# Performance work log

Measured on AMD Instinct MI355X. Metric: run time of the kernel, lower is better.

## Reference

```python
import jax, jax.numpy as jnp
import numpy as np

DIM = 1024
EXPANSION = 4
NUM_EXPERTS = 8
N_TOKENS = 4096
CAPACITY_FACTOR = 1.0  # also becomes the gate's k -> top-1 (bug-faithful)
EPS = 1e-6


def setup_inputs() -> dict:
    key = jax.random.key(0)
    ks = jax.random.split(key, 7)
    h = DIM * EXPANSION
    s = 0.02
    return {
        "x": jax.random.normal(ks[0], (N_TOKENS, DIM), dtype=jnp.float32),
        "w_gate": jax.random.normal(ks[1], (DIM, NUM_EXPERTS), dtype=jnp.float32) * s,
        "b_gate": jnp.zeros((NUM_EXPERTS,), dtype=jnp.float32),
        "w1": jax.random.normal(ks[2], (NUM_EXPERTS, DIM, h), dtype=jnp.float32) * s,
        "b1": jnp.zeros((NUM_EXPERTS, h), dtype=jnp.float32),
        "w2": jax.random.normal(ks[3], (NUM_EXPERTS, h, DIM), dtype=jnp.float32) * s,
        "b2": jnp.zeros((NUM_EXPERTS, DIM), dtype=jnp.float32),
    }


def fast_gelu(x):
    return x * jax.nn.sigmoid(1.702 * x)


def switch_gate(x, w_gate, b_gate):
    # x: [n, d] -> gate_scores: [n, e]
    gate_scores = jax.nn.softmax(x @ w_gate + b_gate, axis=-1)
    capacity = int(CAPACITY_FACTOR * x.shape[0])
    k = int(CAPACITY_FACTOR)  # SwitchMoE passes capacity_factor as k -> top-1
    _, top_k_idx = jax.lax.top_k(gate_scores, k)  # [n, k]
    mask = jnp.zeros_like(gate_scores).at[
        jnp.arange(x.shape[0])[:, None], top_k_idx
    ].set(1.0)
    masked = gate_scores * mask
    denom = masked.sum(axis=0, keepdims=True) + EPS  # [1, e]
    gate_scores = masked / denom * capacity
    # aux loss (use_aux_loss=True in SwitchMoE)
    load = gate_scores.sum(axis=0)               # [e]
    importance = gate_scores.sum(axis=1).mean()  # scalar
    loss = jnp.mean((load - importance) ** 2)
    return gate_scores, loss


def reference(x, w_gate, b_gate, w1, b1, w2, b2):
    gate_scores, loss = switch_gate(x, w_gate, b_gate)  # [n, e], scalar
    # dense compute-all-experts (faithful to the naive module)
    h = fast_gelu(jnp.einsum("nd,edh->enh", x, w1) + b1[:, None, :])  # [e, n, h]
    expert_out = jnp.einsum("enh,ehd->end", h, w2) + b2[:, None, :]   # [e, n, d]
    # weighted combine: sum_e gate[n,e] * expert_out[e,n,d]
    moe_output = jnp.einsum("ne,end->nd", gate_scores, expert_out)
    return moe_output, loss
```

## Files before the change

### kernel.cpp

```cpp
#include <hip/hip_runtime.h>
#include <hip/hip_bf16.h>
#include <math.h>

#define DIMK   1024
#define HDIM   4096
#define NEXP   8
#define NTOK   4096
#define EPSV   1e-6f

typedef __attribute__((ext_vector_type(4))) float  f32x4;
typedef __attribute__((ext_vector_type(8))) __bf16 bf16x8;
typedef __attribute__((ext_vector_type(4))) __bf16 bf16x4;

__device__ __forceinline__ __bf16 f2bf(float f) { return (__bf16)f; }

__global__ void init_kernel(int* counts, int* cursors, float* S) {
    int t = threadIdx.x;
    if (t < NEXP) { counts[t] = 0; cursors[t] = 0; S[t] = 0.0f; }
}

__global__ __launch_bounds__(256) void gate_kernel(
    const float* __restrict__ x, const float* __restrict__ wg,
    const float* __restrict__ bg,
    float* S, int* counts, float* score_top, int* texp)
{
    int wave = threadIdx.x >> 6;
    int lane = threadIdx.x & 63;
    int n = blockIdx.x * 4 + wave;
    const float* xr = x + (size_t)n * DIMK;

    float acc[NEXP];
#pragma unroll
    for (int e = 0; e < NEXP; e++) acc[e] = 0.0f;

    for (int d = lane; d < DIMK; d += 64) {
        float xv = xr[d];
        const float* wr = wg + (size_t)d * NEXP;
#pragma unroll
        for (int e = 0; e < NEXP; e++) acc[e] += xv * wr[e];
    }
#pragma unroll
    for (int e = 0; e < NEXP; e++) {
#pragma unroll
        for (int off = 32; off > 0; off >>= 1)
            acc[e] += __shfl_down(acc[e], off, 64);
    }
    if (lane == 0) {
        float l[NEXP];
        float m = -1e30f;
#pragma unroll
        for (int e = 0; e < NEXP; e++) { l[e] = acc[e] + bg[e]; m = fmaxf(m, l[e]); }
        float p[NEXP]; float s = 0.0f;
#pragma unroll
        for (int e = 0; e < NEXP; e++) { p[e] = expf(l[e] - m); s += p[e]; }
        int best = 0; float bv = p[0];
#pragma unroll
        for (int e = 1; e < NEXP; e++) if (p[e] > bv) { bv = p[e]; best = e; }
        float sc = bv / s;
        score_top[n] = sc;
        texp[n] = best;
        atomicAdd(&S[best], sc);
        atomicAdd(&counts[best], 1);
    }
}

__global__ void finalize_kernel(const float* S, const int* counts,
                                int* offsets, float* loss_out)
{
    if (threadIdx.x == 0 && blockIdx.x == 0) {
        int off = 0;
        float loadv[NEXP]; float tot = 0.0f;
        for (int e = 0; e < NEXP; e++) { offsets[e] = off; off += counts[e]; }
        for (int e = 0; e < NEXP; e++) {
            loadv[e] = S[e] / (S[e] + EPSV) * (float)NTOK;
            tot += loadv[e];
        }
        float imp = tot / (float)NTOK;
        float loss = 0.0f;
        for (int e = 0; e < NEXP; e++) { float d = loadv[e] - imp; loss += d * d; }
        loss_out[0] = loss / (float)NEXP;
    }
}

__global__ __launch_bounds__(256) void assign_kernel(
    const int* __restrict__ texp, const float* __restrict__ score_top,
    const float* __restrict__ S, const int* __restrict__ offsets,
    int* cursors, int* perm, float* gatew)
{
    int n = blockIdx.x * 256 + threadIdx.x;
    int e = texp[n];
    int pos = atomicAdd(&cursors[e], 1);
    perm[offsets[e] + pos] = n;
    gatew[n] = score_top[n] / (S[e] + EPSV) * (float)NTOK;
}

__global__ __launch_bounds__(256) void gemm1_kernel(
    const float* __restrict__ x, const float* __restrict__ w1,
    const float* __restrict__ b1,
    const int* __restrict__ perm, const int* __restrict__ counts,
    const int* __restrict__ offsets, __bf16* __restrict__ hbuf)
{
    int bx  = blockIdx.x;
    int e   = bx >> 10;
    int rem = bx & 1023;
    int mt  = rem >> 5;
    int nt  = rem & 31;
    int ce  = counts[e];
    int m0  = mt * 128;
    if (m0 >= ce) return;
    int off = offsets[e];
    int n0  = nt * 128;
    const float* B = w1 + (size_t)e * DIMK * HDIM;

    __shared__ __bf16 As[128][40];
    __shared__ __bf16 Bs[128][40];

    int t = threadIdx.x;

    const float* aptr[4];
#pragma unroll
    for (int i = 0; i < 4; i++) {
        int r  = (t >> 3) + 32 * i;
        int ri = m0 + r; if (ri >= ce) ri = ce - 1;
        aptr[i] = x + (size_t)perm[off + ri] * DIMK;
    }
    int ac4 = (t & 7) * 4;

    int bj = t & 127;
    int bgp = t >> 7;
    const float* bcol = B + n0 + bj;

    int lane = t & 63;
    int wv   = t >> 6;
    int wm   = (wv >> 1) * 64;
    int wn   = (wv & 1) * 64;
    int lr   = lane & 15;
    int lq   = lane >> 4;

    f32x4 acc[4][4];
#pragma unroll
    for (int mi = 0; mi < 4; mi++)
#pragma unroll
        for (int ni = 0; ni < 4; ni++) acc[mi][ni] = (f32x4)0.0f;

    for (int k0 = 0; k0 < DIMK; k0 += 32) {
#pragma unroll
        for (int i = 0; i < 4; i++) {
            int r = (t >> 3) + 32 * i;
            f32x4 v = *(const f32x4*)(aptr[i] + k0 + ac4);
            bf16x4 s4 = { f2bf(v.x), f2bf(v.y), f2bf(v.z), f2bf(v.w) };
            *(bf16x4*)&As[r][ac4] = s4;
        }
#pragma unroll
        for (int i = 0; i < 4; i++) {
            int kk = bgp * 4 + i * 8;
            const float* p = bcol + (size_t)(k0 + kk) * HDIM;
            bf16x4 s4 = { f2bf(p[0]), f2bf(p[HDIM]),
                          f2bf(p[2 * HDIM]), f2bf(p[3 * HDIM]) };
            *(bf16x4*)&Bs[bj][kk] = s4;
        }
        __syncthreads();

        bf16x8 af[4], bfr[4];
#pragma unroll
        for (int i = 0; i < 4; i++) {
            af[i]  = *(const bf16x8*)&As[wm + i * 16 + lr][lq * 8];
            bfr[i] = *(const bf16x8*)&Bs[wn + i * 16 + lr][lq * 8];
        }
#pragma unroll
        for (int mi = 0; mi < 4; mi++)
#pragma unroll
            for (int ni = 0; ni < 4; ni++)
                acc[mi][ni] = __builtin_amdgcn_mfma_f32_16x16x32_bf16(
                    af[mi], bfr[ni], acc[mi][ni], 0, 0, 0);
        __syncthreads();
    }

    const float* b1e = b1 + (size_t)e * HDIM;
#pragma unroll
    for (int mi = 0; mi < 4; mi++) {
#pragma unroll
        for (int r = 0; r < 4; r++) {
            int i = m0 + wm + mi * 16 + lq * 4 + r;
            if (i < ce) {
                __bf16* hrow = hbuf + (size_t)(off + i) * HDIM;
#pragma unroll
                for (int ni = 0; ni < 4; ni++) {
                    int j = n0 + wn + ni * 16 + lr;
                    float v = acc[mi][ni][r] + b1e[j];
                    v = v / (1.0f + __expf(-1.702f * v));
                    hrow[j] = f2bf(v);
                }
            }
        }
    }
}

__global__ __launch_bounds__(256) void gemm2_kernel(
    const __bf16* __restrict__ hbuf, const float* __restrict__ w2,
    const float* __restrict__ b2,
    const int* __restrict__ perm, const int* __restrict__ counts,
    const int* __restrict__ offsets, const float* __restrict__ gatew,
    float* __restrict__ out)
{
    int bx  = blockIdx.x;
    int e   = bx >> 9;
    int rem = bx & 511;
    int mt  = rem >> 3;
    int nt  = rem & 7;
    int ce  = counts[e];
    int m0  = mt * 64;
    if (m0 >= ce) return;
    int off = offsets[e];
    int n0  = nt * 128;
    const float* B = w2 + (size_t)e * HDIM * DIMK;

    __shared__ __bf16 As[64][40];
    __shared__ __bf16 Bs[128][40];

    int t = threadIdx.x;

    int ar = t >> 2;
    int ac8 = (t & 3) * 8;
    {
        int ri = m0 + ar; if (ri >= ce) ri = ce - 1;
        ar = ar;
    }
    int ri0 = m0 + ar; if (ri0 >= ce) ri0 = ce - 1;
    const __bf16* aptr = hbuf + (size_t)(off + ri0) * HDIM;

    int bj = t & 127;
    int bgp = t >> 7;
    const float* bcol = B + n0 + bj;

    int lane = t & 63;
    int wv   = t >> 6;
    int wm   = (wv >> 1) * 32;
    int wn   = (wv & 1) * 64;
    int lr   = lane & 15;
    int lq   = lane >> 4;

    f32x4 acc[2][4];
#pragma unroll
    for (int mi = 0; mi < 2; mi++)
#pragma unroll
        for (int ni = 0; ni < 4; ni++) acc[mi][ni] = (f32x4)0.0f;

    for (int k0 = 0; k0 < HDIM; k0 += 32) {
        {
            bf16x8 v = *(const bf16x8*)(aptr + k0 + ac8);
            *(bf16x8*)&As[ar][ac8] = v;
        }
#pragma unroll
        for (int i = 0; i < 4; i++) {
            int kk = bgp * 4 + i * 8;
            const float* p = bcol + (size_t)(k0 + kk) * DIMK;
            bf16x4 s4 = { f2bf(p[0]), f2bf(p[DIMK]),
                          f2bf(p[2 * DIMK]), f2bf(p[3 * DIMK]) };
            *(bf16x4*)&Bs[bj][kk] = s4;
        }
        __syncthreads();

        bf16x8 af[2], bfr[4];
#pragma unroll
        for (int i = 0; i < 2; i++)
            af[i] = *(const bf16x8*)&As[wm + i * 16 + lr][lq * 8];
#pragma unroll
        for (int i = 0; i < 4; i++)
            bfr[i] = *(const bf16x8*)&Bs[wn + i * 16 + lr][lq * 8];
#pragma unroll
        for (int mi = 0; mi < 2; mi++)
#pragma unroll
            for (int ni = 0; ni < 4; ni++)
                acc[mi][ni] = __builtin_amdgcn_mfma_f32_16x16x32_bf16(
                    af[mi], bfr[ni], acc[mi][ni], 0, 0, 0);
        __syncthreads();
    }

    const float* b2e = b2 + (size_t)e * DIMK;
#pragma unroll
    for (int mi = 0; mi < 2; mi++) {
#pragma unroll
        for (int r = 0; r < 4; r++) {
            int i = m0 + wm + mi * 16 + lq * 4 + r;
            if (i < ce) {
                int tok = perm[off + i];
                float g = gatew[tok];
                float* orow = out + (size_t)tok * DIMK;
#pragma unroll
                for (int ni = 0; ni < 4; ni++) {
                    int j = n0 + wn + ni * 16 + lr;
                    orow[j] = (acc[mi][ni][r] + b2e[j]) * g;
                }
            }
        }
    }
}

extern "C" void kernel_launch(void* const* d_in, const int* in_sizes, int n_in,
                              void* d_out, int out_size, void* d_ws, size_t ws_size,
                              hipStream_t stream)
{
    const float* x  = (const float*)d_in[0];
    const float* wg = (const float*)d_in[1];
    const float* bg = (const float*)d_in[2];
    const float* w1 = (const float*)d_in[3];
    const float* b1 = (const float*)d_in[4];
    const float* w2 = (const float*)d_in[5];
    const float* b2 = (const float*)d_in[6];
    float* out = (float*)d_out;

    char* wsb = (char*)d_ws;
    int*   counts  = (int*)  (wsb + 0);
    int*   cursors = (int*)  (wsb + 32);
    int*   offsets = (int*)  (wsb + 64);
    float* S       = (float*)(wsb + 96);
    float* score   = (float*)(wsb + 128);
    int*   texp    = (int*)  (wsb + 16512);
    int*   perm    = (int*)  (wsb + 32896);
    float* gatew   = (float*)(wsb + 49280);
    __bf16* hbuf   = (__bf16*)(wsb + 131072);

    init_kernel<<<1, 64, 0, stream>>>(counts, cursors, S);
    gate_kernel<<<NTOK / 4, 256, 0, stream>>>(x, wg, bg, S, counts, score, texp);
    finalize_kernel<<<1, 64, 0, stream>>>(S, counts, offsets, out + (size_t)NTOK * DIMK);
    assign_kernel<<<NTOK / 256, 256, 0, stream>>>(texp, score, S, offsets,
                                                  cursors, perm, gatew);
    gemm1_kernel<<<NEXP * 32 * 32, 256, 0, stream>>>(x, w1, b1, perm, counts,
                                                     offsets, hbuf);
    gemm2_kernel<<<NEXP * 64 * 8, 256, 0, stream>>>(hbuf, w2, b2, perm, counts,
                                                    offsets, gatew, out);
}
```

Before: 630.9 us.

## Vectorize weight loads, split-K gemm2 with atomic combine, rework gate kernel

Gate kernel now uses one block per token with vectorized x and w_gate loads and a shared-memory reduction. Both GEMMs load B tiles as float4 row pairs instead of strided scalar column reads, which gives coalesced fp32 weight traffic. gemm2 gets a 64-wide K tile and a two-way split-K. Partial results are combined with atomicAdd into an output pre-filled with the gate-weighted bias by a new bias_init kernel. This adds atomic traffic and makes the summation order nondeterministic.

```diff
diff --git a/kernel.cpp b/kernel.cpp
--- a/kernel.cpp
+++ b/kernel.cpp
@@ -11,6 +11,7 @@
 typedef __attribute__((ext_vector_type(4))) float  f32x4;
 typedef __attribute__((ext_vector_type(8))) __bf16 bf16x8;
 typedef __attribute__((ext_vector_type(4))) __bf16 bf16x4;
+typedef __attribute__((ext_vector_type(2))) __bf16 bf16x2;
 
 __device__ __forceinline__ __bf16 f2bf(float f) { return (__bf16)f; }
 
@@ -24,38 +25,47 @@
     const float* __restrict__ bg,
     float* S, int* counts, float* score_top, int* texp)
 {
-    int wave = threadIdx.x >> 6;
-    int lane = threadIdx.x & 63;
-    int n = blockIdx.x * 4 + wave;
-    const float* xr = x + (size_t)n * DIMK;
-
-    float acc[NEXP];
-#pragma unroll
-    for (int e = 0; e < NEXP; e++) acc[e] = 0.0f;
-
-    for (int d = lane; d < DIMK; d += 64) {
-        float xv = xr[d];
-        const float* wr = wg + (size_t)d * NEXP;
-#pragma unroll
-        for (int e = 0; e < NEXP; e++) acc[e] += xv * wr[e];
+    int n = blockIdx.x;
+    int t = threadIdx.x;
+    f32x4 xv = *(const f32x4*)(x + (size_t)n * DIMK + t * 4);
+
+    float p[NEXP];
+#pragma unroll
+    for (int e = 0; e < NEXP; e++) p[e] = 0.0f;
+#pragma unroll
+    for (int j = 0; j < 4; j++) {
+        int d = t * 4 + j;
+        f32x4 wa = *(const f32x4*)(wg + (size_t)d * NEXP);
+        f32x4 wb = *(const f32x4*)(wg + (size_t)d * NEXP + 4);
+#pragma unroll
+        for (int e = 0; e < 4; e++) { p[e] += xv[j] * wa[e]; p[e + 4] += xv[j] * wb[e]; }
     }
 #pragma unroll
     for (int e = 0; e < NEXP; e++) {
 #pragma unroll
         for (int off = 32; off > 0; off >>= 1)
-            acc[e] += __shfl_down(acc[e], off, 64);
-    }
+            p[e] += __shfl_down(p[e], off, 64);
+    }
+    __shared__ float red[4][NEXP];
+    int lane = t & 63, wv = t >> 6;
     if (lane == 0) {
-        float l[NEXP];
-        float m = -1e30f;
-#pragma unroll
-        for (int e = 0; e < NEXP; e++) { l[e] = acc[e] + bg[e]; m = fmaxf(m, l[e]); }
-        float p[NEXP]; float s = 0.0f;
-#pragma unroll
-        for (int e = 0; e < NEXP; e++) { p[e] = expf(l[e] - m); s += p[e]; }
-        int best = 0; float bv = p[0];
-#pragma unroll
-        for (int e = 1; e < NEXP; e++) if (p[e] > bv) { bv = p[e]; best = e; }
+#pragma unroll
+        for (int e = 0; e < NEXP; e++) red[wv][e] = p[e];
+    }
+    __syncthreads();
+    if (t == 0) {
+        float l[NEXP]; float m = -1e30f;
+#pragma unroll
+        for (int e = 0; e < NEXP; e++) {
+            l[e] = red[0][e] + red[1][e] + red[2][e] + red[3][e] + bg[e];
+            m = fmaxf(m, l[e]);
+        }
+        float pe[NEXP]; float s = 0.0f;
+#pragma unroll
+        for (int e = 0; e < NEXP; e++) { pe[e] = __expf(l[e] - m); s += pe[e]; }
+        int best = 0; float bv = pe[0];
+#pragma unroll
+        for (int e = 1; e < NEXP; e++) if (pe[e] > bv) { bv = pe[e]; best = e; }
         float sc = bv / s;
         score_top[n] = sc;
         texp[n] = best;
@@ -92,6 +102,19 @@
     int pos = atomicAdd(&cursors[e], 1);
     perm[offsets[e] + pos] = n;
     gatew[n] = score_top[n] / (S[e] + EPSV) * (float)NTOK;
+}
+
+__global__ __launch_bounds__(256) void bias_init_kernel(
+    const int* __restrict__ texp, const float* __restrict__ gatew,
+    const float* __restrict__ b2, float* __restrict__ out)
+{
+    int n = blockIdx.x;
+    int t = threadIdx.x;
+    int e = texp[n];
+    float g = gatew[n];
+    f32x4 b = *(const f32x4*)(b2 + (size_t)e * DIMK + t * 4);
+    f32x4 o = { b.x * g, b.y * g, b.z * g, b.w * g };
+    *(f32x4*)(out + (size_t)n * DIMK + t * 4) = o;
 }
 
 __global__ __launch_bounds__(256) void gemm1_kernel(
@@ -121,14 +144,14 @@
 #pragma unroll
     for (int i = 0; i < 4; i++) {
         int r  = (t >> 3) + 32 * i;
-        int ri = m0 + r; if (ri >= ce) ri = ce - 1;
+        int ri = (m0 + r < ce) ? (m0 + r) : (ce - 1);
         aptr[i] = x + (size_t)perm[off + ri] * DIMK;
     }
     int ac4 = (t & 7) * 4;
 
-    int bj = t & 127;
-    int bgp = t >> 7;
-    const float* bcol = B + n0 + bj;
+    int n4 = ((t >> 3) & 31) * 4;
+    int kp = t & 7;
+    const float* Bb = B + n0 + n4;
 
     int lane = t & 63;
     int wv   = t >> 6;
@@ -152,12 +175,16 @@
             *(bf16x4*)&As[r][ac4] = s4;
         }
 #pragma unroll
-        for (int i = 0; i < 4; i++) {
-            int kk = bgp * 4 + i * 8;
-            const float* p = bcol + (size_t)(k0 + kk) * HDIM;
-            bf16x4 s4 = { f2bf(p[0]), f2bf(p[HDIM]),
-                          f2bf(p[2 * HDIM]), f2bf(p[3 * HDIM]) };
-            *(bf16x4*)&Bs[bj][kk] = s4;
+        for (int i = 0; i < 2; i++) {
+            int p = kp + 8 * i;
+            const float* p0 = Bb + (size_t)(k0 + 2 * p) * HDIM;
+            f32x4 v0 = *(const f32x4*)p0;
+            f32x4 v1 = *(const f32x4*)(p0 + HDIM);
+#pragma unroll
+            for (int j = 0; j < 4; j++) {
+                bf16x2 w = { f2bf(v0[j]), f2bf(v1[j]) };
+                *(bf16x2*)&Bs[n4 + j][2 * p] = w;
+            }
         }
         __syncthreads();
 
@@ -198,14 +225,15 @@
 
 __global__ __launch_bounds__(256) void gemm2_kernel(
     const __bf16* __restrict__ hbuf, const float* __restrict__ w2,
-    const float* __restrict__ b2,
     const int* __restrict__ perm, const int* __restrict__ counts,
     const int* __restrict__ offsets, const float* __restrict__ gatew,
     float* __restrict__ out)
 {
     int bx  = blockIdx.x;
-    int e   = bx >> 9;
-    int rem = bx & 511;
+    int sk  = bx & 1;
+    int rest = bx >> 1;
+    int e   = rest >> 9;
+    int rem = rest & 511;
     int mt  = rem >> 3;
     int nt  = rem & 7;
     int ce  = counts[e];
@@ -215,23 +243,23 @@
     int n0  = nt * 128;
     const float* B = w2 + (size_t)e * HDIM * DIMK;
 
-    __shared__ __bf16 As[64][40];
-    __shared__ __bf16 Bs[128][40];
-
-    int t = threadIdx.x;
-
-    int ar = t >> 2;
-    int ac8 = (t & 3) * 8;
-    {
-        int ri = m0 + ar; if (ri >= ce) ri = ce - 1;
-        ar = ar;
-    }
-    int ri0 = m0 + ar; if (ri0 >= ce) ri0 = ce - 1;
-    const __bf16* aptr = hbuf + (size_t)(off + ri0) * HDIM;
-
-    int bj = t & 127;
-    int bgp = t >> 7;
-    const float* bcol = B + n0 + bj;
+    __shared__ __bf16 As[64][72];
+    __shared__ __bf16 Bs[128][72];
+
+    int t = threadIdx.x;
+
+    const __bf16* aptr[2];
+#pragma unroll
+    for (int i = 0; i < 2; i++) {
+        int r  = (t >> 3) + 32 * i;
+        int ri = (m0 + r < ce) ? (m0 + r) : (ce - 1);
+        aptr[i] = hbuf + (size_t)(off + ri) * HDIM;
+    }
+    int ac8 = (t & 7) * 8;
+
+    int n4 = ((t >> 3) & 31) * 4;
+    int kp = t & 7;
+    const float* Bb = B + n0 + n4;
 
     int lane = t & 63;
     int wv   = t >> 6;
@@ -246,38 +274,48 @@
 #pragma unroll
         for (int ni = 0; ni < 4; ni++) acc[mi][ni] = (f32x4)0.0f;
 
-    for (int k0 = 0; k0 < HDIM; k0 += 32) {
-        {
-            bf16x8 v = *(const bf16x8*)(aptr + k0 + ac8);
-            *(bf16x8*)&As[ar][ac8] = v;
+    int kbeg = sk * (HDIM / 2);
+    int kend = kbeg + HDIM / 2;
+    for (int k0 = kbeg; k0 < kend; k0 += 64) {
+#pragma unroll
+        for (int i = 0; i < 2; i++) {
+            int r = (t >> 3) + 32 * i;
+            bf16x8 v = *(const bf16x8*)(aptr[i] + k0 + ac8);
+            *(bf16x8*)&As[r][ac8] = v;
         }
 #pragma unroll
         for (int i = 0; i < 4; i++) {
-            int kk = bgp * 4 + i * 8;
-            const float* p = bcol + (size_t)(k0 + kk) * DIMK;
-            bf16x4 s4 = { f2bf(p[0]), f2bf(p[DIMK]),
-                          f2bf(p[2 * DIMK]), f2bf(p[3 * DIMK]) };
-            *(bf16x4*)&Bs[bj][kk] = s4;
+            int p = kp + 8 * i;
+            const float* p0 = Bb + (size_t)(k0 + 2 * p) * DIMK;
+            f32x4 v0 = *(const f32x4*)p0;
+            f32x4 v1 = *(const f32x4*)(p0 + DIMK);
+#pragma unroll
+            for (int j = 0; j < 4; j++) {
+                bf16x2 w = { f2bf(v0[j]), f2bf(v1[j]) };
+                *(bf16x2*)&Bs[n4 + j][2 * p] = w;
+            }
         }
         __syncthreads();
 
-        bf16x8 af[2], bfr[4];
-#pragma unroll
-        for (int i = 0; i < 2; i++)
-            af[i] = *(const bf16x8*)&As[wm + i * 16 + lr][lq * 8];
-#pragma unroll
-        for (int i = 0; i < 4; i++)
-            bfr[i] = *(const bf16x8*)&Bs[wn + i * 16 + lr][lq * 8];
-#pragma unroll
-        for (int mi = 0; mi < 2; mi++)
-#pragma unroll
-            for (int ni = 0; ni < 4; ni++)
-                acc[mi][ni] = __builtin_amdgcn_mfma_f32_16x16x32_bf16(
-                    af[mi], bfr[ni], acc[mi][ni], 0, 0, 0);
+#pragma unroll
+        for (int ks = 0; ks < 2; ks++) {
+            bf16x8 af[2], bfr[4];
+#pragma unroll
+            for (int i = 0; i < 2; i++)
+                af[i] = *(const bf16x8*)&As[wm + i * 16 + lr][lq * 8 + ks * 32];
+#pragma unroll
+            for (int i = 0; i < 4; i++)
+                bfr[i] = *(const bf16x8*)&Bs[wn + i * 16 + lr][lq * 8 + ks * 32];
+#pragma unroll
+            for (int mi = 0; mi < 2; mi++)
+#pragma unroll
+                for (int ni = 0; ni < 4; ni++)
+                    acc[mi][ni] = __builtin_amdgcn_mfma_f32_16x16x32_bf16(
+                        af[mi], bfr[ni], acc[mi][ni], 0, 0, 0);
+        }
         __syncthreads();
     }
 
-    const float* b2e = b2 + (size_t)e * DIMK;
 #pragma unroll
     for (int mi = 0; mi < 2; mi++) {
 #pragma unroll
@@ -290,7 +328,7 @@
 #pragma unroll
                 for (int ni = 0; ni < 4; ni++) {
                     int j = n0 + wn + ni * 16 + lr;
-                    orow[j] = (acc[mi][ni][r] + b2e[j]) * g;
+                    atomicAdd(&orow[j], acc[mi][ni][r] * g);
                 }
             }
         }
@@ -322,12 +360,13 @@
     __bf16* hbuf   = (__bf16*)(wsb + 131072);
 
     init_kernel<<<1, 64, 0, stream>>>(counts, cursors, S);
-    gate_kernel<<<NTOK / 4, 256, 0, stream>>>(x, wg, bg, S, counts, score, texp);
+    gate_kernel<<<NTOK, 256, 0, stream>>>(x, wg, bg, S, counts, score, texp);
     finalize_kernel<<<1, 64, 0, stream>>>(S, counts, offsets, out + (size_t)NTOK * DIMK);
     assign_kernel<<<NTOK / 256, 256, 0, stream>>>(texp, score, S, offsets,
                                                   cursors, perm, gatew);
+    bias_init_kernel<<<NTOK, 256, 0, stream>>>(texp, gatew, b2, out);
     gemm1_kernel<<<NEXP * 32 * 32, 256, 0, stream>>>(x, w1, b1, perm, counts,
                                                      offsets, hbuf);
-    gemm2_kernel<<<NEXP * 64 * 8, 256, 0, stream>>>(hbuf, w2, b2, perm, counts,
-                                                    offsets, gatew, out);
-}
+    gemm2_kernel<<<NEXP * 64 * 8 * 2, 256, 0, stream>>>(hbuf, w2, perm, counts,
+                                                        offsets, gatew, out);
+}
```

New measurement: 603.5 us. -4.4%, faster.
